# Performance work log

Measured on AMD Instinct MI355X. Metric: run time of the kernel, lower is better.

## Reference

```python
import jax, jax.numpy as jnp
import numpy as np

B, C, H, W = 2, 256, 96, 96
CQ = C // 8  # q/k channel dim = 32


def setup_inputs() -> dict:
    key = jax.random.key(0)
    k1, k2, k3 = jax.random.split(key, 3)
    x = jax.random.normal(k1, (B, C, H, W), dtype=jnp.float32)
    # 1x1 conv weight [out=2*C/8+C, in=C] (spectral_norm is a weight
    # parametrization; post-normalization the forward is a plain 1x1 conv,
    # so we treat w as the already-normalized weight). Scaled ~ unit sigma.
    w = jax.random.normal(k2, (2 * CQ + C, C), dtype=jnp.float32) * 0.05
    gamma = jax.random.normal(k3, (1,), dtype=jnp.float32)
    return {"x": x, "w": w, "gamma": gamma}


def reference(x, w, gamma):
    b, c, h, wd = x.shape
    n = h * wd
    xf = x.reshape(b, c, n)                      # [B, C, N]
    qkv = jnp.einsum('oc,bcn->bon', w, xf)       # 1x1 conv == channel matmul
    q = qkv[:, :CQ]                              # [B, C/8, N]
    k = qkv[:, CQ:2 * CQ]                        # [B, C/8, N]
    v = qkv[:, 2 * CQ:]                          # [B, C,   N]
    scores = jnp.einsum('bdi,bdj->bij', q, k)    # [B, N, N] = q^T k
    attn = jax.nn.softmax(scores, axis=1)        # softmax over i (dim=1)
    o = jnp.einsum('bci,bij->bcj', v, attn)      # [B, C, N]
    return (gamma * o).reshape(b, c, h, wd) + x
```

## Files before the change

### kernel.cpp

```cpp
#include <hip/hip_runtime.h>
#include <hip/hip_bf16.h>

#define NTOK 9216
#define CCH  256
#define DQK  32
#define BJ   128
#define SSEG 8

typedef __attribute__((ext_vector_type(8))) short short8;
typedef __attribute__((ext_vector_type(4))) float f32x4;
typedef __attribute__((ext_vector_type(16))) float f32x16;

__device__ __forceinline__ unsigned short f2bf(float x) {
    union { float f; unsigned int u; } v; v.f = x;
    return (unsigned short)((v.u + 0x7FFF + ((v.u >> 16) & 1)) >> 16);
}
__device__ __forceinline__ float bf2f(unsigned short h) {
    union { unsigned int u; float f; } v; v.u = ((unsigned int)h) << 16; return v.f;
}

#if __has_builtin(__builtin_amdgcn_cvt_pk_bf16_f32)
__device__ __forceinline__ unsigned int pack2bf(float a, float b) {
    auto p = __builtin_amdgcn_cvt_pk_bf16_f32(a, b);
    union { decltype(p) v; unsigned int u; } cv; cv.v = p; return cv.u;
}
#else
__device__ __forceinline__ unsigned int pack2bf(float a, float b) {
    return (unsigned)f2bf(a) | ((unsigned)f2bf(b) << 16);
}
#endif

#if __has_builtin(__builtin_amdgcn_exp2f)
#define EXP2(x) __builtin_amdgcn_exp2f(x)
#else
#define EXP2(x) __expf((x) * 0.69314718055994531f)
#endif

#define GLOAD_LDS16(g, l)                                                     \
    __builtin_amdgcn_global_load_lds(                                         \
        (const __attribute__((address_space(1))) unsigned int*)(g),           \
        (__attribute__((address_space(3))) unsigned int*)(l), 16, 0, 0)

__device__ __forceinline__ f32x16 zero16() {
    f32x16 z;
#pragma unroll
    for (int i = 0; i < 16; ++i) z[i] = 0.f;
    return z;
}

__global__ __launch_bounds__(256) void wcvt_kernel(
    const float* __restrict__ w, unsigned short* __restrict__ wbf)
{
    const int i = (blockIdx.x * 256 + threadIdx.x) * 4;
    f32x4 v = *(const f32x4*)(w + i);
    *(unsigned int*)(wbf + i)     = pack2bf(v[0], v[1]);
    *(unsigned int*)(wbf + i + 2) = pack2bf(v[2], v[3]);
}

__global__ __launch_bounds__(256) void qkv_kernel(
    const float* __restrict__ x, const unsigned short* __restrict__ wbf,
    unsigned short* __restrict__ qT, unsigned short* __restrict__ kT,
    unsigned short* __restrict__ vcn)
{
    const int id   = blockIdx.x;
    const int b    = id & 1;
    const int n0   = (id >> 1) * 16;
    const int t    = threadIdx.x;
    const int wv   = t >> 6;
    const int lane = t & 63;
    const int l15  = lane & 15;
    const int qd   = lane >> 4;

    const float* xb = x + (size_t)b * CCH * NTOK + n0 + l15;

    f32x4 acc[5];
#pragma unroll
    for (int tt = 0; tt < 5; ++tt) acc[tt] = (f32x4){0.f, 0.f, 0.f, 0.f};

    const unsigned short* wrow = wbf + (size_t)(80 * wv + l15) * CCH + qd * 8;

#pragma unroll
    for (int kk = 0; kk < 8; ++kk) {
        float xe[8];
#pragma unroll
        for (int e = 0; e < 8; ++e)
            xe[e] = xb[(size_t)(32 * kk + 8 * qd + e) * NTOK];
        short8 bfr;
#pragma unroll
        for (int e = 0; e < 8; ++e)
            bfr[e] = (short)f2bf(xe[e]);
#pragma unroll
        for (int tt = 0; tt < 5; ++tt) {
            short8 afr = *(const short8*)(wrow + (size_t)(16 * tt) * CCH + 32 * kk);
            acc[tt] = __builtin_amdgcn_mfma_f32_16x16x32_bf16(afr, bfr, acc[tt], 0, 0, 0);
        }
    }

    const int n = n0 + l15;
    const float L2E = 1.44269504088896f;
#pragma unroll
    for (int tt = 0; tt < 5; ++tt) {
        const int o0l = 80 * wv + 16 * tt + 4 * qd;
        if (o0l < 32) {
            unsigned short* d = qT + ((size_t)b * NTOK + n) * DQK + o0l;
            *(unsigned int*)d       = pack2bf(acc[tt][0] * L2E, acc[tt][1] * L2E);
            *(unsigned int*)(d + 2) = pack2bf(acc[tt][2] * L2E, acc[tt][3] * L2E);
        } else if (o0l < 64) {
            unsigned short* d = kT + ((size_t)b * NTOK + n) * DQK + (o0l - 32);
            *(unsigned int*)d       = pack2bf(acc[tt][0], acc[tt][1]);
            *(unsigned int*)(d + 2) = pack2bf(acc[tt][2], acc[tt][3]);
        } else {
            unsigned short* d = vcn + ((size_t)b * CCH + (o0l - 64)) * NTOK + n;
            d[0] = f2bf(acc[tt][0]);
            d[(size_t)NTOK] = f2bf(acc[tt][1]);
            d[(size_t)2 * NTOK] = f2bf(acc[tt][2]);
            d[(size_t)3 * NTOK] = f2bf(acc[tt][3]);
        }
    }
}

__global__ __launch_bounds__(256, 3) void attn_partial_kernel(
    const unsigned short* __restrict__ qT, const unsigned short* __restrict__ kT,
    const unsigned short* __restrict__ vcn,
    unsigned short* __restrict__ Opart, float* __restrict__ lpart)
{
    __shared__ __align__(16) unsigned short Vt[2][128 * 64];
    __shared__ __align__(16) unsigned short Qt[2][64 * 32];

    const int id    = blockIdx.x;
    const int combo = id & 15;
    const int s     = combo >> 1;
    const int cb    = combo & 1;
    const int r     = id >> 4;
    const int jb    = r % 72;
    const int b     = r / 72;

    const int t    = threadIdx.x;
    const int wv   = t >> 6;
    const int lane = t & 63;
    const int l31  = lane & 31;
    const int b5   = lane >> 5;
    const int jw   = jb * BJ + 32 * wv;
    const int c0   = cb * 128;
    const int iBeg = s * (NTOK / SSEG);
    const int iEnd = iBeg + (NTOK / SSEG);

    short8 kf[2];
#pragma unroll
    for (int kd = 0; kd < 2; ++kd)
        kf[kd] = *(const short8*)(kT + ((size_t)b * NTOK + jw + l31) * DQK + 16 * kd + 8 * b5);

    f32x16 acc[4];
#pragma unroll
    for (int ct = 0; ct < 4; ++ct) acc[ct] = zero16();
    float lw = 0.f;

    const unsigned short* vsegb = vcn + ((size_t)b * CCH + c0) * NTOK;
    const unsigned short* qsegb = qT + (size_t)b * NTOK * DQK;

    auto stage = [&](int buf, int i0s) {
        const int vrow = 8 * wv + (lane >> 3);
        const int vsl  = ((lane & 7) ^ (vrow & 7)) * 8;
#pragma unroll
        for (int g = 0; g < 4; ++g) {
            const unsigned short* src =
                vsegb + (size_t)(32 * g + vrow) * NTOK + i0s + vsl;
            GLOAD_LDS16(src, &Vt[buf][(32 * g + 8 * wv) * 64]);
        }
        const int qrow = 16 * wv + (lane >> 2);
        const int qsl  = ((lane & 3) ^ (qrow & 3)) * 8;
        const unsigned short* qsrc = qsegb + (size_t)(i0s + qrow) * DQK + qsl;
        GLOAD_LDS16(qsrc, &Qt[buf][(16 * wv) * 32]);
    };

    int cur = 0;
    stage(0, iBeg);
    __syncthreads();

#pragma unroll 1
    for (int i0 = iBeg; i0 < iEnd; i0 += 64) {
        const int inext = (i0 + 64 < iEnd) ? i0 + 64 : iBeg;
        stage(cur ^ 1, inext);

#pragma unroll
        for (int it = 0; it < 2; ++it) {
            short8 af0 = *(const short8*)&Qt[cur][(32 * it + l31) * 32 +
                            (((b5) ^ (l31 & 3)) << 3)];
            short8 af1 = *(const short8*)&Qt[cur][(32 * it + l31) * 32 +
                            (((2 + b5) ^ (l31 & 3)) << 3)];
            short8 vf[2][4];
#pragma unroll
            for (int kc2 = 0; kc2 < 2; ++kc2)
#pragma unroll
                for (int ct = 0; ct < 4; ++ct)
                    vf[kc2][ct] = *(const short8*)&Vt[cur][(32 * ct + l31) * 64 +
                        (((4 * it + 2 * kc2 + b5) ^ (l31 & 7)) << 3)];

            __builtin_amdgcn_s_setprio(1);
            f32x16 sc = __builtin_amdgcn_mfma_f32_32x32x16_bf16(af0, kf[0], zero16(), 0, 0, 0);
            sc = __builtin_amdgcn_mfma_f32_32x32x16_bf16(af1, kf[1], sc, 0, 0, 0);
            __builtin_amdgcn_s_setprio(0);

            unsigned int pk[8];
            float ls = 0.f;
#pragma unroll
            for (int w = 0; w < 8; ++w) {
                float p0 = EXP2(sc[2 * w]);
                float p1 = EXP2(sc[2 * w + 1]);
                ls += p0 + p1;
                pk[w] = pack2bf(p0, p1);
            }
            lw += ls;

#pragma unroll
            for (int kc2 = 0; kc2 < 2; ++kc2) {
                const int base = 4 * kc2;
                unsigned int m1 = b5 ? pk[base]     : pk[base + 2];
                unsigned int m2 = b5 ? pk[base + 1] : pk[base + 3];
                unsigned int x1 = __shfl_xor(m1, 32);
                unsigned int x2 = __shfl_xor(m2, 32);
                unsigned int wd0 = b5 ? x1 : pk[base];
                unsigned int wd1 = b5 ? x2 : pk[base + 1];
                unsigned int wd2 = b5 ? pk[base + 2] : x1;
                unsigned int wd3 = b5 ? pk[base + 3] : x2;
                union { unsigned int u[4]; short8 s8; } bu;
                bu.u[0] = wd0; bu.u[1] = wd1; bu.u[2] = wd2; bu.u[3] = wd3;
                __builtin_amdgcn_s_setprio(1);
#pragma unroll
                for (int ct = 0; ct < 4; ++ct)
                    acc[ct] = __builtin_amdgcn_mfma_f32_32x32x16_bf16(
                        vf[kc2][ct], bu.s8, acc[ct], 0, 0, 0);
                __builtin_amdgcn_s_setprio(0);
            }
        }
        __syncthreads();
        cur ^= 1;
    }

    float lt = lw + __shfl_xor(lw, 32);
    if (cb == 0 && lane < 32)
        lpart[(size_t)(s * 2 + b) * NTOK + jw + l31] = lt;

#pragma unroll
    for (int ct = 0; ct < 4; ++ct)
#pragma unroll
        for (int w = 0; w < 16; ++w) {
            const int c = c0 + 32 * ct + (w & 3) + 8 * (w >> 2) + 4 * b5;
            Opart[((size_t)(s * 2 + b) * CCH + c) * NTOK + jw + l31] = f2bf(acc[ct][w]);
        }
}

__global__ __launch_bounds__(256) void reduce_kernel(
    const unsigned short* __restrict__ Opart, const float* __restrict__ lpart,
    const float* __restrict__ x, const float* __restrict__ gamma,
    float* __restrict__ out)
{
    const size_t flat = ((size_t)blockIdx.x * 256 + threadIdx.x) * 4;
    const int j = (int)(flat % NTOK);
    const int b = (int)(flat / ((size_t)CCH * NTOK));
    const size_t inb = flat - (size_t)b * CCH * NTOK;

    f32x4 o = {0.f, 0.f, 0.f, 0.f};
    f32x4 l = {0.f, 0.f, 0.f, 0.f};
#pragma unroll
    for (int s = 0; s < SSEG; ++s) {
        const size_t plane = (size_t)(s * 2 + b) * CCH * NTOK;
        unsigned long long ov = *(const unsigned long long*)(Opart + plane + inb);
        f32x4 lv = *(const f32x4*)(lpart + (size_t)(s * 2 + b) * NTOK + j);
        o[0] += bf2f((unsigned short)(ov));
        o[1] += bf2f((unsigned short)(ov >> 16));
        o[2] += bf2f((unsigned short)(ov >> 32));
        o[3] += bf2f((unsigned short)(ov >> 48));
        l[0] += lv[0]; l[1] += lv[1]; l[2] += lv[2]; l[3] += lv[3];
    }
    const float g = gamma[0];
    f32x4 xv = *(const f32x4*)(x + flat);
    f32x4 rr;
    rr[0] = g * o[0] / l[0] + xv[0];
    rr[1] = g * o[1] / l[1] + xv[1];
    rr[2] = g * o[2] / l[2] + xv[2];
    rr[3] = g * o[3] / l[3] + xv[3];
    *(f32x4*)(out + flat) = rr;
}

extern "C" void kernel_launch(void* const* d_in, const int* in_sizes, int n_in,
                              void* d_out, int out_size, void* d_ws, size_t ws_size,
                              hipStream_t stream) {
    const float* x     = (const float*)d_in[0];
    const float* w     = (const float*)d_in[1];
    const float* gamma = (const float*)d_in[2];
    float* out = (float*)d_out;

    unsigned short* qT  = (unsigned short*)d_ws;
    unsigned short* kT  = qT + (size_t)2 * NTOK * DQK;
    unsigned short* vcn = kT + (size_t)2 * NTOK * DQK;
    unsigned short* Opart = vcn + (size_t)2 * CCH * NTOK;
    float* lpart = (float*)(Opart + (size_t)SSEG * 2 * CCH * NTOK);
    unsigned short* wbf = (unsigned short*)(lpart + (size_t)SSEG * 2 * NTOK);

    wcvt_kernel<<<80, 256, 0, stream>>>(w, wbf);

    qkv_kernel<<<1152, 256, 0, stream>>>(x, wbf, qT, kT, vcn);

    attn_partial_kernel<<<2304, 256, 0, stream>>>(qT, kT, vcn, Opart, lpart);

    reduce_kernel<<<(unsigned)((size_t)2 * CCH * NTOK / 4 / 256), 256, 0, stream>>>(
        Opart, lpart, x, gamma, out);
}
```

Baseline: 262.0 us.

## Double per-wave j tile to reuse staged V/Q across two column groups

Each wave now handles 64 output columns (two 32-column groups) instead of 32. Every V and Q fragment loaded from LDS therefore feeds twice as many MFMAs, and the grid halves to 1152 blocks. The LDS layout for V is split per 32-token sub-tile, and the cross-half exchange uses permlane32_swap where the builtin exists. The cost is doubled accumulator registers, so occupancy drops from 3 to 2 blocks per CU and fewer blocks are left to cover latency.

```diff
diff --git a/kernel.cpp b/kernel.cpp
--- a/kernel.cpp
+++ b/kernel.cpp
@@ -4,12 +4,12 @@
 #define NTOK 9216
 #define CCH  256
 #define DQK  32
-#define BJ   128
 #define SSEG 8
 
 typedef __attribute__((ext_vector_type(8))) short short8;
 typedef __attribute__((ext_vector_type(4))) float f32x4;
 typedef __attribute__((ext_vector_type(16))) float f32x16;
+typedef __attribute__((ext_vector_type(2))) unsigned int uint2v;
 
 __device__ __forceinline__ unsigned short f2bf(float x) {
     union { float f; unsigned int u; } v; v.f = x;
@@ -119,12 +119,12 @@
     }
 }
 
-__global__ __launch_bounds__(256, 3) void attn_partial_kernel(
+__global__ __launch_bounds__(256, 2) void attn_partial_kernel(
     const unsigned short* __restrict__ qT, const unsigned short* __restrict__ kT,
     const unsigned short* __restrict__ vcn,
     unsigned short* __restrict__ Opart, float* __restrict__ lpart)
 {
-    __shared__ __align__(16) unsigned short Vt[2][128 * 64];
+    __shared__ __align__(16) unsigned short Vt[2][2][128 * 32];
     __shared__ __align__(16) unsigned short Qt[2][64 * 32];
 
     const int id    = blockIdx.x;
@@ -132,45 +132,52 @@
     const int s     = combo >> 1;
     const int cb    = combo & 1;
     const int r     = id >> 4;
-    const int jb    = r % 72;
-    const int b     = r / 72;
+    const int jb    = r % 36;
+    const int b     = r / 36;
 
     const int t    = threadIdx.x;
     const int wv   = t >> 6;
     const int lane = t & 63;
     const int l31  = lane & 31;
     const int b5   = lane >> 5;
-    const int jw   = jb * BJ + 32 * wv;
+    const int jw   = jb * 256 + 64 * wv;
     const int c0   = cb * 128;
     const int iBeg = s * (NTOK / SSEG);
     const int iEnd = iBeg + (NTOK / SSEG);
 
-    short8 kf[2];
-#pragma unroll
-    for (int kd = 0; kd < 2; ++kd)
-        kf[kd] = *(const short8*)(kT + ((size_t)b * NTOK + jw + l31) * DQK + 16 * kd + 8 * b5);
-
-    f32x16 acc[4];
-#pragma unroll
-    for (int ct = 0; ct < 4; ++ct) acc[ct] = zero16();
-    float lw = 0.f;
+    short8 kf[2][2];
+#pragma unroll
+    for (int jg = 0; jg < 2; ++jg)
+#pragma unroll
+        for (int kd = 0; kd < 2; ++kd)
+            kf[jg][kd] = *(const short8*)(kT +
+                ((size_t)b * NTOK + jw + 32 * jg + l31) * DQK + 16 * kd + 8 * b5);
+
+    f32x16 acc[2][4];
+#pragma unroll
+    for (int jg = 0; jg < 2; ++jg)
+#pragma unroll
+        for (int ct = 0; ct < 4; ++ct) acc[jg][ct] = zero16();
+    float lw[2] = {0.f, 0.f};
 
     const unsigned short* vsegb = vcn + ((size_t)b * CCH + c0) * NTOK;
     const unsigned short* qsegb = qT + (size_t)b * NTOK * DQK;
 
     auto stage = [&](int buf, int i0s) {
-        const int vrow = 8 * wv + (lane >> 3);
-        const int vsl  = ((lane & 7) ^ (vrow & 7)) * 8;
-#pragma unroll
-        for (int g = 0; g < 4; ++g) {
-            const unsigned short* src =
-                vsegb + (size_t)(32 * g + vrow) * NTOK + i0s + vsl;
-            GLOAD_LDS16(src, &Vt[buf][(32 * g + 8 * wv) * 64]);
-        }
-        const int qrow = 16 * wv + (lane >> 2);
-        const int qsl  = ((lane & 3) ^ (qrow & 3)) * 8;
-        const unsigned short* qsrc = qsegb + (size_t)(i0s + qrow) * DQK + qsl;
-        GLOAD_LDS16(qsrc, &Qt[buf][(16 * wv) * 32]);
+#pragma unroll
+        for (int it = 0; it < 2; ++it)
+#pragma unroll
+            for (int h = 0; h < 2; ++h) {
+                const int c = 32 * wv + 16 * h + (lane >> 2);
+                const int u = (lane & 3) ^ (c & 3);
+                const unsigned short* src =
+                    vsegb + (size_t)c * NTOK + i0s + 32 * it + 8 * u;
+                GLOAD_LDS16(src, &Vt[buf][it][(32 * wv + 16 * h) * 32]);
+            }
+        const int qr = 16 * wv + (lane >> 2);
+        const int qu = (lane & 3) ^ (qr & 3);
+        GLOAD_LDS16(qsegb + (size_t)(i0s + qr) * DQK + 8 * qu,
+                    &Qt[buf][(16 * wv) * 32]);
     };
 
     int cur = 0;
@@ -184,70 +191,92 @@
 
 #pragma unroll
         for (int it = 0; it < 2; ++it) {
-            short8 af0 = *(const short8*)&Qt[cur][(32 * it + l31) * 32 +
-                            (((b5) ^ (l31 & 3)) << 3)];
-            short8 af1 = *(const short8*)&Qt[cur][(32 * it + l31) * 32 +
-                            (((2 + b5) ^ (l31 & 3)) << 3)];
+            const int qrow = (32 * it + l31) * 32;
+            short8 af0 = *(const short8*)&Qt[cur][qrow + 8 * ((b5) ^ (l31 & 3))];
+            short8 af1 = *(const short8*)&Qt[cur][qrow + 8 * ((2 + b5) ^ (l31 & 3))];
             short8 vf[2][4];
 #pragma unroll
             for (int kc2 = 0; kc2 < 2; ++kc2)
 #pragma unroll
                 for (int ct = 0; ct < 4; ++ct)
-                    vf[kc2][ct] = *(const short8*)&Vt[cur][(32 * ct + l31) * 64 +
-                        (((4 * it + 2 * kc2 + b5) ^ (l31 & 7)) << 3)];
-
+                    vf[kc2][ct] = *(const short8*)&Vt[cur][it][
+                        (32 * ct + l31) * 32 + 8 * ((2 * kc2 + b5) ^ (l31 & 3))];
+
+            f32x16 sc0, sc1;
             __builtin_amdgcn_s_setprio(1);
-            f32x16 sc = __builtin_amdgcn_mfma_f32_32x32x16_bf16(af0, kf[0], zero16(), 0, 0, 0);
-            sc = __builtin_amdgcn_mfma_f32_32x32x16_bf16(af1, kf[1], sc, 0, 0, 0);
+            sc0 = __builtin_amdgcn_mfma_f32_32x32x16_bf16(af0, kf[0][0], zero16(), 0, 0, 0);
+            sc0 = __builtin_amdgcn_mfma_f32_32x32x16_bf16(af1, kf[0][1], sc0, 0, 0, 0);
+            sc1 = __builtin_amdgcn_mfma_f32_32x32x16_bf16(af0, kf[1][0], zero16(), 0, 0, 0);
+            sc1 = __builtin_amdgcn_mfma_f32_32x32x16_bf16(af1, kf[1][1], sc1, 0, 0, 0);
             __builtin_amdgcn_s_setprio(0);
 
-            unsigned int pk[8];
-            float ls = 0.f;
-#pragma unroll
-            for (int w = 0; w < 8; ++w) {
-                float p0 = EXP2(sc[2 * w]);
-                float p1 = EXP2(sc[2 * w + 1]);
-                ls += p0 + p1;
-                pk[w] = pack2bf(p0, p1);
-            }
-            lw += ls;
-
-#pragma unroll
-            for (int kc2 = 0; kc2 < 2; ++kc2) {
-                const int base = 4 * kc2;
-                unsigned int m1 = b5 ? pk[base]     : pk[base + 2];
-                unsigned int m2 = b5 ? pk[base + 1] : pk[base + 3];
-                unsigned int x1 = __shfl_xor(m1, 32);
-                unsigned int x2 = __shfl_xor(m2, 32);
-                unsigned int wd0 = b5 ? x1 : pk[base];
-                unsigned int wd1 = b5 ? x2 : pk[base + 1];
-                unsigned int wd2 = b5 ? pk[base + 2] : x1;
-                unsigned int wd3 = b5 ? pk[base + 3] : x2;
-                union { unsigned int u[4]; short8 s8; } bu;
-                bu.u[0] = wd0; bu.u[1] = wd1; bu.u[2] = wd2; bu.u[3] = wd3;
-                __builtin_amdgcn_s_setprio(1);
-#pragma unroll
-                for (int ct = 0; ct < 4; ++ct)
-                    acc[ct] = __builtin_amdgcn_mfma_f32_32x32x16_bf16(
-                        vf[kc2][ct], bu.s8, acc[ct], 0, 0, 0);
-                __builtin_amdgcn_s_setprio(0);
+#pragma unroll
+            for (int jg = 0; jg < 2; ++jg) {
+                const f32x16 sc = jg ? sc1 : sc0;
+                unsigned int pk[8];
+                float ls = 0.f;
+#pragma unroll
+                for (int w = 0; w < 8; ++w) {
+                    float p0 = EXP2(sc[2 * w]);
+                    float p1 = EXP2(sc[2 * w + 1]);
+                    ls += p0 + p1;
+                    pk[w] = pack2bf(p0, p1);
+                }
+                lw[jg] += ls;
+
+#pragma unroll
+                for (int kc2 = 0; kc2 < 2; ++kc2) {
+                    const int base = 4 * kc2;
+                    union { unsigned int u[4]; short8 s8; } bu;
+#if __has_builtin(__builtin_amdgcn_permlane32_swap)
+                    uint2v r1 = __builtin_amdgcn_permlane32_swap(
+                        pk[base], pk[base + 2], false, false);
+                    uint2v r2 = __builtin_amdgcn_permlane32_swap(
+                        pk[base + 1], pk[base + 3], false, false);
+                    bu.u[0] = r1[0]; bu.u[1] = r2[0];
+                    bu.u[2] = r1[1]; bu.u[3] = r2[1];
+#else
+                    unsigned int m1 = b5 ? pk[base]     : pk[base + 2];
+                    unsigned int m2 = b5 ? pk[base + 1] : pk[base + 3];
+                    unsigned int x1 = __shfl_xor(m1, 32);
+                    unsigned int x2 = __shfl_xor(m2, 32);
+                    bu.u[0] = b5 ? x1 : pk[base];
+                    bu.u[1] = b5 ? x2 : pk[base + 1];
+                    bu.u[2] = b5 ? pk[base + 2] : x1;
+                    bu.u[3] = b5 ? pk[base + 3] : x2;
+#endif
+                    __builtin_amdgcn_s_setprio(1);
+#pragma unroll
+                    for (int ct = 0; ct < 4; ++ct)
+                        acc[jg][ct] = __builtin_amdgcn_mfma_f32_32x32x16_bf16(
+                            vf[kc2][ct], bu.s8, acc[jg][ct], 0, 0, 0);
+                    __builtin_amdgcn_s_setprio(0);
+                }
             }
         }
         __syncthreads();
         cur ^= 1;
     }
 
-    float lt = lw + __shfl_xor(lw, 32);
-    if (cb == 0 && lane < 32)
-        lpart[(size_t)(s * 2 + b) * NTOK + jw + l31] = lt;
-
-#pragma unroll
-    for (int ct = 0; ct < 4; ++ct)
-#pragma unroll
-        for (int w = 0; w < 16; ++w) {
-            const int c = c0 + 32 * ct + (w & 3) + 8 * (w >> 2) + 4 * b5;
-            Opart[((size_t)(s * 2 + b) * CCH + c) * NTOK + jw + l31] = f2bf(acc[ct][w]);
+    if (cb == 0) {
+        float lt0 = lw[0] + __shfl_xor(lw[0], 32);
+        float lt1 = lw[1] + __shfl_xor(lw[1], 32);
+        if (b5 == 0) {
+            lpart[(size_t)(s * 2 + b) * NTOK + jw + l31]      = lt0;
+            lpart[(size_t)(s * 2 + b) * NTOK + jw + 32 + l31] = lt1;
         }
+    }
+
+#pragma unroll
+    for (int jg = 0; jg < 2; ++jg)
+#pragma unroll
+        for (int ct = 0; ct < 4; ++ct)
+#pragma unroll
+            for (int w = 0; w < 16; ++w) {
+                const int c = c0 + 32 * ct + (w & 3) + 8 * (w >> 2) + 4 * b5;
+                Opart[((size_t)(s * 2 + b) * CCH + c) * NTOK + jw + 32 * jg + l31] =
+                    f2bf(acc[jg][ct][w]);
+            }
 }
 
 __global__ __launch_bounds__(256) void reduce_kernel(
@@ -302,7 +331,7 @@
 
     qkv_kernel<<<1152, 256, 0, stream>>>(x, wbf, qT, kT, vcn);
 
-    attn_partial_kernel<<<2304, 256, 0, stream>>>(qT, kT, vcn, Opart, lpart);
+    attn_partial_kernel<<<1152, 256, 0, stream>>>(qT, kT, vcn, Opart, lpart);
 
     reduce_kernel<<<(unsigned)((size_t)2 * CCH * NTOK / 4 / 256), 256, 0, stream>>>(
         Opart, lpart, x, gamma, out);
```

After: 500.7 us. 91.1% more time.

## Use permlane32_swap for P exchange, reorder V loads, relayout Q tile in LDS

Applied to the files above, without the earlier changes.

Swaps the two __shfl_xor plus select sequence for the half-wave exchange of packed probabilities for the permlane32_swap builtin when it is available. This avoids LDS-routed shuffles and removes the selects. It also moves the V fragment reads inside the kc2 loop to lower register pressure. The Q tile in LDS gets a new layout of 32 rows by 64 with its own swizzle, and the V staging rows are reassigned so each wave loads a contiguous 32-row block. The risks are correctness of the new Q addressing and whether the builtin exists on this toolchain.

```diff
diff --git a/kernel.cpp b/kernel.cpp
--- a/kernel.cpp
+++ b/kernel.cpp
@@ -4,12 +4,12 @@
 #define NTOK 9216
 #define CCH  256
 #define DQK  32
-#define BJ   128
 #define SSEG 8
 
 typedef __attribute__((ext_vector_type(8))) short short8;
 typedef __attribute__((ext_vector_type(4))) float f32x4;
 typedef __attribute__((ext_vector_type(16))) float f32x16;
+typedef __attribute__((ext_vector_type(2))) unsigned int uint2v;
 
 __device__ __forceinline__ unsigned short f2bf(float x) {
     union { float f; unsigned int u; } v; v.f = x;
@@ -125,7 +125,7 @@
     unsigned short* __restrict__ Opart, float* __restrict__ lpart)
 {
     __shared__ __align__(16) unsigned short Vt[2][128 * 64];
-    __shared__ __align__(16) unsigned short Qt[2][64 * 32];
+    __shared__ __align__(16) unsigned short Qt[2][32 * 64];
 
     const int id    = blockIdx.x;
     const int combo = id & 15;
@@ -140,7 +140,7 @@
     const int lane = t & 63;
     const int l31  = lane & 31;
     const int b5   = lane >> 5;
-    const int jw   = jb * BJ + 32 * wv;
+    const int jw   = jb * 128 + 32 * wv;
     const int c0   = cb * 128;
     const int iBeg = s * (NTOK / SSEG);
     const int iEnd = iBeg + (NTOK / SSEG);
@@ -148,7 +148,8 @@
     short8 kf[2];
 #pragma unroll
     for (int kd = 0; kd < 2; ++kd)
-        kf[kd] = *(const short8*)(kT + ((size_t)b * NTOK + jw + l31) * DQK + 16 * kd + 8 * b5);
+        kf[kd] = *(const short8*)(kT +
+            ((size_t)b * NTOK + jw + l31) * DQK + 16 * kd + 8 * b5);
 
     f32x16 acc[4];
 #pragma unroll
@@ -159,18 +160,18 @@
     const unsigned short* qsegb = qT + (size_t)b * NTOK * DQK;
 
     auto stage = [&](int buf, int i0s) {
-        const int vrow = 8 * wv + (lane >> 3);
-        const int vsl  = ((lane & 7) ^ (vrow & 7)) * 8;
 #pragma unroll
         for (int g = 0; g < 4; ++g) {
+            const int rv = 32 * wv + 8 * g + (lane >> 3);
             const unsigned short* src =
-                vsegb + (size_t)(32 * g + vrow) * NTOK + i0s + vsl;
-            GLOAD_LDS16(src, &Vt[buf][(32 * g + 8 * wv) * 64]);
-        }
-        const int qrow = 16 * wv + (lane >> 2);
-        const int qsl  = ((lane & 3) ^ (qrow & 3)) * 8;
-        const unsigned short* qsrc = qsegb + (size_t)(i0s + qrow) * DQK + qsl;
-        GLOAD_LDS16(qsrc, &Qt[buf][(16 * wv) * 32]);
+                vsegb + (size_t)rv * NTOK + i0s + 8 * ((lane & 7) ^ (rv & 7));
+            GLOAD_LDS16(src, &Vt[buf][(32 * wv + 8 * g) * 64]);
+        }
+        const int rq = 8 * wv + (lane >> 3);
+        const int iq = 2 * rq + ((lane & 7) >> 2);
+        const int cq = (lane & 3) ^ (rq & 3);
+        GLOAD_LDS16(qsegb + (size_t)(i0s + iq) * DQK + 8 * cq,
+                    &Qt[buf][(8 * wv) * 64]);
     };
 
     int cur = 0;
@@ -184,52 +185,65 @@
 
 #pragma unroll
         for (int it = 0; it < 2; ++it) {
-            short8 af0 = *(const short8*)&Qt[cur][(32 * it + l31) * 32 +
-                            (((b5) ^ (l31 & 3)) << 3)];
-            short8 af1 = *(const short8*)&Qt[cur][(32 * it + l31) * 32 +
-                            (((2 + b5) ^ (l31 & 3)) << 3)];
-            short8 vf[2][4];
-#pragma unroll
-            for (int kc2 = 0; kc2 < 2; ++kc2)
+            const int qoff = (16 * it + (l31 >> 1)) * 64 + 32 * (l31 & 1);
+            const int qswz = (l31 >> 1) & 3;
+            short8 af0 = *(const short8*)&Qt[cur][qoff + 8 * ((b5) ^ qswz)];
+            short8 af1 = *(const short8*)&Qt[cur][qoff + 8 * ((2 + b5) ^ qswz)];
+
+            unsigned int pk[8];
+            {
+                __builtin_amdgcn_s_setprio(1);
+                f32x16 sc = __builtin_amdgcn_mfma_f32_32x32x16_bf16(af0, kf[0], zero16(), 0, 0, 0);
+                sc = __builtin_amdgcn_mfma_f32_32x32x16_bf16(af1, kf[1], sc, 0, 0, 0);
+                __builtin_amdgcn_s_setprio(0);
+                float ls = 0.f;
+#pragma unroll
+                for (int w = 0; w < 8; ++w) {
+                    float p0 = EXP2(sc[2 * w]);
+                    float p1 = EXP2(sc[2 * w + 1]);
+                    ls += p0 + p1;
+                    pk[w] = pack2bf(p0, p1);
+                }
+                lw += ls;
+            }
+
+#pragma unroll
+            for (int kc2 = 0; kc2 < 2; ++kc2) {
+                short8 vf[4];
 #pragma unroll
                 for (int ct = 0; ct < 4; ++ct)
-                    vf[kc2][ct] = *(const short8*)&Vt[cur][(32 * ct + l31) * 64 +
-                        (((4 * it + 2 * kc2 + b5) ^ (l31 & 7)) << 3)];
-
-            __builtin_amdgcn_s_setprio(1);
-            f32x16 sc = __builtin_amdgcn_mfma_f32_32x32x16_bf16(af0, kf[0], zero16(), 0, 0, 0);
-            sc = __builtin_amdgcn_mfma_f32_32x32x16_bf16(af1, kf[1], sc, 0, 0, 0);
-            __builtin_amdgcn_s_setprio(0);
-
-            unsigned int pk[8];
-            float ls = 0.f;
-#pragma unroll
-            for (int w = 0; w < 8; ++w) {
-                float p0 = EXP2(sc[2 * w]);
-                float p1 = EXP2(sc[2 * w + 1]);
-                ls += p0 + p1;
-                pk[w] = pack2bf(p0, p1);
-            }
-            lw += ls;
-
-#pragma unroll
-            for (int kc2 = 0; kc2 < 2; ++kc2) {
+                    vf[ct] = *(const short8*)&Vt[cur][
+                        (32 * ct + l31) * 64 +
+                        8 * ((4 * it + 2 * kc2 + b5) ^ (l31 & 7))];
+
                 const int base = 4 * kc2;
-                unsigned int m1 = b5 ? pk[base]     : pk[base + 2];
-                unsigned int m2 = b5 ? pk[base + 1] : pk[base + 3];
-                unsigned int x1 = __shfl_xor(m1, 32);
-                unsigned int x2 = __shfl_xor(m2, 32);
-                unsigned int wd0 = b5 ? x1 : pk[base];
-                unsigned int wd1 = b5 ? x2 : pk[base + 1];
-                unsigned int wd2 = b5 ? pk[base + 2] : x1;
-                unsigned int wd3 = b5 ? pk[base + 3] : x2;
                 union { unsigned int u[4]; short8 s8; } bu;
-                bu.u[0] = wd0; bu.u[1] = wd1; bu.u[2] = wd2; bu.u[3] = wd3;
+#if __has_builtin(__builtin_amdgcn_permlane32_swap)
+                {
+                    uint2v r1 = __builtin_amdgcn_permlane32_swap(
+                        pk[base], pk[base + 2], false, false);
+                    uint2v r2 = __builtin_amdgcn_permlane32_swap(
+                        pk[base + 1], pk[base + 3], false, false);
+                    bu.u[0] = r1[0]; bu.u[1] = r2[0];
+                    bu.u[2] = r1[1]; bu.u[3] = r2[1];
+                }
+#else
+                {
+                    unsigned int m1 = b5 ? pk[base]     : pk[base + 2];
+                    unsigned int m2 = b5 ? pk[base + 1] : pk[base + 3];
+                    unsigned int x1 = __shfl_xor(m1, 32);
+                    unsigned int x2 = __shfl_xor(m2, 32);
+                    bu.u[0] = b5 ? x1 : pk[base];
+                    bu.u[1] = b5 ? x2 : pk[base + 1];
+                    bu.u[2] = b5 ? pk[base + 2] : x1;
+                    bu.u[3] = b5 ? pk[base + 3] : x2;
+                }
+#endif
                 __builtin_amdgcn_s_setprio(1);
 #pragma unroll
                 for (int ct = 0; ct < 4; ++ct)
                     acc[ct] = __builtin_amdgcn_mfma_f32_32x32x16_bf16(
-                        vf[kc2][ct], bu.s8, acc[ct], 0, 0, 0);
+                        vf[ct], bu.s8, acc[ct], 0, 0, 0);
                 __builtin_amdgcn_s_setprio(0);
             }
         }
@@ -237,16 +251,19 @@
         cur ^= 1;
     }
 
-    float lt = lw + __shfl_xor(lw, 32);
-    if (cb == 0 && lane < 32)
-        lpart[(size_t)(s * 2 + b) * NTOK + jw + l31] = lt;
+    if (cb == 0) {
+        float lt = lw + __shfl_xor(lw, 32);
+        if (b5 == 0)
+            lpart[(size_t)(s * 2 + b) * NTOK + jw + l31] = lt;
+    }
 
 #pragma unroll
     for (int ct = 0; ct < 4; ++ct)
 #pragma unroll
         for (int w = 0; w < 16; ++w) {
             const int c = c0 + 32 * ct + (w & 3) + 8 * (w >> 2) + 4 * b5;
-            Opart[((size_t)(s * 2 + b) * CCH + c) * NTOK + jw + l31] = f2bf(acc[ct][w]);
+            Opart[((size_t)(s * 2 + b) * CCH + c) * NTOK + jw + l31] =
+                f2bf(acc[ct][w]);
         }
 }
 
```

After: 249.0 us, median of 2. -5.0%, faster.
